# Kernel optimization log

Measured on AMD Instinct MI355X. Metric: run time of the kernel, lower is better.

Reference implementation:

```python
import jax, jax.numpy as jnp
import numpy as np

N_NODES = 50000
N_EDGES = 800000
D = 64


def setup_inputs() -> dict:
    key = jax.random.key(0)
    ks = jax.random.split(key, 8)
    x = jax.random.normal(ks[0], (N_NODES, D), dtype=jnp.float32)
    edge_index = jax.random.randint(ks[1], (2, N_EDGES), 0, N_NODES, dtype=jnp.int64)
    # GCNConv params (PyG: Linear without bias inside lin, bias added after aggregation)
    def glorot(k, fan_in, fan_out):
        lim = (6.0 / (fan_in + fan_out)) ** 0.5
        return jax.random.uniform(k, (fan_in, fan_out), jnp.float32, -lim, lim)
    W1 = glorot(ks[2], D, D); b1 = jnp.zeros((D,), jnp.float32)
    W2 = glorot(ks[3], D, D); b2 = jnp.zeros((D,), jnp.float32)
    W3 = glorot(ks[4], D, D); b3 = jnp.zeros((D,), jnp.float32)
    return {"x": x, "edge_index": edge_index,
            "W1": W1, "b1": b1, "W2": W2, "b2": b2, "W3": W3, "b3": b3}


def _gcn_norm(edge_index, n_nodes, dtype):
    # Add self-loops, compute symmetric normalization D^-1/2 (A+I) D^-1/2 (PyG GCNConv default).
    loop = jnp.arange(n_nodes, dtype=edge_index.dtype)
    src = jnp.concatenate([edge_index[0], loop])  # message source j
    dst = jnp.concatenate([edge_index[1], loop])  # aggregation target i
    deg = jax.ops.segment_sum(jnp.ones_like(dst, dtype=dtype), dst, num_segments=n_nodes)
    dinv = jnp.where(deg > 0, jax.lax.rsqrt(deg), 0.0)
    norm = dinv[src] * dinv[dst]  # [E + N]
    return src, dst, norm


def _gcn_conv(x, src, dst, norm, W, b, n_nodes):
    h = x @ W                              # [N, D_out]
    msg = h[src] * norm[:, None]           # gather + scale, [E+N, D_out]
    out = jax.ops.segment_sum(msg, dst, num_segments=n_nodes)  # scatter-add
    return out + b


def reference(x, edge_index, W1, b1, W2, b2, W3, b3):
    n = x.shape[0]
    src, dst, norm = _gcn_norm(edge_index, n, x.dtype)
    # layer 0: conv -> relu -> residual
    h = _gcn_conv(x, src, dst, norm, W1, b1, n)
    h = jax.nn.relu(h) + x
    # layer 1: conv -> relu -> residual
    r = h
    h = _gcn_conv(h, src, dst, norm, W2, b2, n)
    h = jax.nn.relu(h) + r
    # layer 2 (final): conv only
    h = _gcn_conv(h, src, dst, norm, W3, b3, n)
    return h
```

## Files before the change

### kernel.cpp

```cpp
#include <hip/hip_runtime.h>
#include <hip/hip_bf16.h>


#define CAP 64
#define EDGE_CHUNK 1024

typedef __attribute__((ext_vector_type(8))) short bf16x8;
typedef __attribute__((ext_vector_type(4))) float f32x4;

__device__ inline unsigned pack_bf16(float a, float b) {
    union { float f; unsigned i; } ua, ub;
    ua.f = a; ub.f = b;
    unsigned x = (ua.i + 0x7fffu + ((ua.i >> 16) & 1u)) >> 16;
    unsigned y = (ub.i + 0x7fffu + ((ub.i >> 16) & 1u)) >> 16;
    return x | (y << 16);
}
__device__ inline unsigned short to_bf16(float a) {
    union { float f; unsigned i; } u; u.f = a;
    return (unsigned short)((u.i + 0x7fffu + ((u.i >> 16) & 1u)) >> 16);
}
__device__ inline void acc_bf16x2(unsigned u, float& a, float& b) {
    union { unsigned i; float f; } lo, hi;
    lo.i = u << 16;
    hi.i = u & 0xffff0000u;
    a += lo.f; b += hi.f;
}

__global__ void fill_kernel(const int* __restrict__ src, const int* __restrict__ dst,
                            int* __restrict__ cnt, int* __restrict__ adj,
                            int E, int npc) {
    int cls = blockIdx.x & 7;
    int base = (blockIdx.x >> 3) * EDGE_CHUNK;
    int end = min(base + EDGE_CHUNK, E);
    int lo = cls * npc, hi = lo + npc;
    for (int e = base + threadIdx.x; e < end; e += blockDim.x) {
        int d = dst[e];
        if (d >= lo && d < hi) {
            int p = atomicAdd(&cnt[d], 1);
            adj[(size_t)d * CAP + p] = src[e];
        }
    }
}

__global__ __launch_bounds__(256) void gemm_kernel(const float* __restrict__ in,
                                                   const float* __restrict__ W,
                                                   const int* __restrict__ cnt,
                                                   unsigned short* __restrict__ g, int n) {
    __shared__ unsigned short Wb[512 * 8];
    int t = threadIdx.x;

#pragma unroll
    for (int e0 = 0; e0 < 2; e0++) {
        int e = t + e0 * 256;
        int sc = e >> 6;
        int l  = e & 63;
        int s = sc >> 2, c = sc & 3;
        int nn = c * 16 + (l & 15);
        int kb = s * 32 + (l >> 4) * 8;
        const float* wp = &W[(size_t)kb * 64 + nn];
        unsigned q0 = pack_bf16(wp[0 * 64], wp[1 * 64]);
        unsigned q1 = pack_bf16(wp[2 * 64], wp[3 * 64]);
        unsigned q2 = pack_bf16(wp[4 * 64], wp[5 * 64]);
        unsigned q3 = pack_bf16(wp[6 * 64], wp[7 * 64]);
        *(uint4*)&Wb[e * 8] = make_uint4(q0, q1, q2, q3);
    }

    int wv = t >> 6;
    int lane = t & 63;
    int quad = lane >> 4;
    int m16 = lane & 15;

    int rowA = blockIdx.x * 64 + wv * 16 + m16;
    union { bf16x8 v; uint4 u; } a0, a1;
    {
        float4 f0 = make_float4(0, 0, 0, 0), f1 = f0, f2 = f0, f3 = f0;
        if (rowA < n) {
            const float* rp = &in[(size_t)rowA * 64];
            f0 = *(const float4*)&rp[quad * 8];
            f1 = *(const float4*)&rp[quad * 8 + 4];
            f2 = *(const float4*)&rp[32 + quad * 8];
            f3 = *(const float4*)&rp[32 + quad * 8 + 4];
        }
        a0.u = make_uint4(pack_bf16(f0.x, f0.y), pack_bf16(f0.z, f0.w),
                          pack_bf16(f1.x, f1.y), pack_bf16(f1.z, f1.w));
        a1.u = make_uint4(pack_bf16(f2.x, f2.y), pack_bf16(f2.z, f2.w),
                          pack_bf16(f3.x, f3.y), pack_bf16(f3.z, f3.w));
    }
    __syncthreads();

    f32x4 acc[4];
#pragma unroll
    for (int c = 0; c < 4; c++) {
        bf16x8 b0 = *(const bf16x8*)&Wb[((size_t)(0 * 4 + c) * 64 + lane) * 8];
        bf16x8 b1 = *(const bf16x8*)&Wb[((size_t)(1 * 4 + c) * 64 + lane) * 8];
        f32x4 z = {0.f, 0.f, 0.f, 0.f};
        z = __builtin_amdgcn_mfma_f32_16x16x32_bf16(a0.v, b0, z, 0, 0, 0);
        z = __builtin_amdgcn_mfma_f32_16x16x32_bf16(a1.v, b1, z, 0, 0, 0);
        acc[c] = z;
    }

    int rowbase = blockIdx.x * 64 + wv * 16 + quad * 4;
    float dv[4];
#pragma unroll
    for (int r = 0; r < 4; r++) {
        int row = rowbase + r;
        dv[r] = (row < n) ? rsqrtf((float)(cnt[row] + 1)) : 0.f;
    }
#pragma unroll
    for (int c = 0; c < 4; c++) {
#pragma unroll
        for (int r = 0; r < 4; r++) {
            int row = rowbase + r;
            if (row < n)
                g[(size_t)row * 64 + c * 16 + m16] = to_bf16(acc[c][r] * dv[r]);
        }
    }
}

template <int MODE>
__global__ __launch_bounds__(256) void agg_kernel(const unsigned short* __restrict__ g,
                                                  const int* __restrict__ cnt,
                                                  const int* __restrict__ adj,
                                                  const float* __restrict__ bias,
                                                  const float* __restrict__ res,
                                                  float* __restrict__ out, int n) {
    int t = threadIdx.x;
    int lg = t & 7;
    int i = blockIdx.x * 32 + (t >> 3);
    if (i >= n) return;
    int deg = cnt[i];
    const int* lst = adj + (size_t)i * CAP;
    const int c8 = lg * 8;
    size_t rowoff = (size_t)i * 64 + c8;
    float4 r0 = make_float4(0.f, 0.f, 0.f, 0.f), r1 = r0;
    if (MODE == 0) {
        r0 = *(const float4*)&res[rowoff];
        r1 = *(const float4*)&res[rowoff + 4];
    }
    float a0 = 0.f, a1 = 0.f, a2 = 0.f, a3 = 0.f;
    float a4 = 0.f, a5 = 0.f, a6 = 0.f, a7 = 0.f;
    {
        uint4 v = *(const uint4*)&g[(size_t)i * 64 + c8];
        acc_bf16x2(v.x, a0, a1); acc_bf16x2(v.y, a2, a3);
        acc_bf16x2(v.z, a4, a5); acc_bf16x2(v.w, a6, a7);
    }
    int k = 0;
    for (; k + 8 <= deg; k += 8) {
        int4 ja = *(const int4*)&lst[k];
        int4 jb = *(const int4*)&lst[k + 4];
        uint4 v0 = *(const uint4*)&g[(size_t)ja.x * 64 + c8];
        uint4 v1 = *(const uint4*)&g[(size_t)ja.y * 64 + c8];
        uint4 v2 = *(const uint4*)&g[(size_t)ja.z * 64 + c8];
        uint4 v3 = *(const uint4*)&g[(size_t)ja.w * 64 + c8];
        uint4 v4 = *(const uint4*)&g[(size_t)jb.x * 64 + c8];
        uint4 v5 = *(const uint4*)&g[(size_t)jb.y * 64 + c8];
        uint4 v6 = *(const uint4*)&g[(size_t)jb.z * 64 + c8];
        uint4 v7 = *(const uint4*)&g[(size_t)jb.w * 64 + c8];
        acc_bf16x2(v0.x, a0, a1); acc_bf16x2(v0.y, a2, a3);
        acc_bf16x2(v0.z, a4, a5); acc_bf16x2(v0.w, a6, a7);
        acc_bf16x2(v1.x, a0, a1); acc_bf16x2(v1.y, a2, a3);
        acc_bf16x2(v1.z, a4, a5); acc_bf16x2(v1.w, a6, a7);
        acc_bf16x2(v2.x, a0, a1); acc_bf16x2(v2.y, a2, a3);
        acc_bf16x2(v2.z, a4, a5); acc_bf16x2(v2.w, a6, a7);
        acc_bf16x2(v3.x, a0, a1); acc_bf16x2(v3.y, a2, a3);
        acc_bf16x2(v3.z, a4, a5); acc_bf16x2(v3.w, a6, a7);
        acc_bf16x2(v4.x, a0, a1); acc_bf16x2(v4.y, a2, a3);
        acc_bf16x2(v4.z, a4, a5); acc_bf16x2(v4.w, a6, a7);
        acc_bf16x2(v5.x, a0, a1); acc_bf16x2(v5.y, a2, a3);
        acc_bf16x2(v5.z, a4, a5); acc_bf16x2(v5.w, a6, a7);
        acc_bf16x2(v6.x, a0, a1); acc_bf16x2(v6.y, a2, a3);
        acc_bf16x2(v6.z, a4, a5); acc_bf16x2(v6.w, a6, a7);
        acc_bf16x2(v7.x, a0, a1); acc_bf16x2(v7.y, a2, a3);
        acc_bf16x2(v7.z, a4, a5); acc_bf16x2(v7.w, a6, a7);
    }
    if (k + 4 <= deg) {
        int4 ja = *(const int4*)&lst[k];
        uint4 v0 = *(const uint4*)&g[(size_t)ja.x * 64 + c8];
        uint4 v1 = *(const uint4*)&g[(size_t)ja.y * 64 + c8];
        uint4 v2 = *(const uint4*)&g[(size_t)ja.z * 64 + c8];
        uint4 v3 = *(const uint4*)&g[(size_t)ja.w * 64 + c8];
        acc_bf16x2(v0.x, a0, a1); acc_bf16x2(v0.y, a2, a3);
        acc_bf16x2(v0.z, a4, a5); acc_bf16x2(v0.w, a6, a7);
        acc_bf16x2(v1.x, a0, a1); acc_bf16x2(v1.y, a2, a3);
        acc_bf16x2(v1.z, a4, a5); acc_bf16x2(v1.w, a6, a7);
        acc_bf16x2(v2.x, a0, a1); acc_bf16x2(v2.y, a2, a3);
        acc_bf16x2(v2.z, a4, a5); acc_bf16x2(v2.w, a6, a7);
        acc_bf16x2(v3.x, a0, a1); acc_bf16x2(v3.y, a2, a3);
        acc_bf16x2(v3.z, a4, a5); acc_bf16x2(v3.w, a6, a7);
        k += 4;
    }
    for (; k < deg; k++) {
        uint4 v = *(const uint4*)&g[(size_t)lst[k] * 64 + c8];
        acc_bf16x2(v.x, a0, a1); acc_bf16x2(v.y, a2, a3);
        acc_bf16x2(v.z, a4, a5); acc_bf16x2(v.w, a6, a7);
    }
    float dv = rsqrtf((float)(deg + 1));
    float4 b0 = *(const float4*)&bias[c8];
    float4 b1 = *(const float4*)&bias[c8 + 4];
    float4 o0, o1;
    o0.x = dv * a0 + b0.x; o0.y = dv * a1 + b0.y;
    o0.z = dv * a2 + b0.z; o0.w = dv * a3 + b0.w;
    o1.x = dv * a4 + b1.x; o1.y = dv * a5 + b1.y;
    o1.z = dv * a6 + b1.z; o1.w = dv * a7 + b1.w;
    if (MODE == 0) {
        o0.x = fmaxf(o0.x, 0.f) + r0.x; o0.y = fmaxf(o0.y, 0.f) + r0.y;
        o0.z = fmaxf(o0.z, 0.f) + r0.z; o0.w = fmaxf(o0.w, 0.f) + r0.w;
        o1.x = fmaxf(o1.x, 0.f) + r1.x; o1.y = fmaxf(o1.y, 0.f) + r1.y;
        o1.z = fmaxf(o1.z, 0.f) + r1.z; o1.w = fmaxf(o1.w, 0.f) + r1.w;
    }
    *(float4*)&out[rowoff] = o0;
    *(float4*)&out[rowoff + 4] = o1;
}

extern "C" void kernel_launch(void* const* d_in, const int* in_sizes, int n_in,
                              void* d_out, int out_size, void* d_ws, size_t ws_size,
                              hipStream_t stream) {
    const float* x  = (const float*)d_in[0];
    const int*   ei = (const int*)d_in[1];
    const float* W1 = (const float*)d_in[2];
    const float* b1 = (const float*)d_in[3];
    const float* W2 = (const float*)d_in[4];
    const float* b2 = (const float*)d_in[5];
    const float* W3 = (const float*)d_in[6];
    const float* b3 = (const float*)d_in[7];
    float* out = (float*)d_out;

    const int N = in_sizes[0] / 64;
    const int E = in_sizes[1] / 2;
    const int* src = ei;
    const int* dst = ei + E;
    const int npc = (N + 7) / 8;
    const int nEdgeChunks = (E + EDGE_CHUNK - 1) / EDGE_CHUNK;

    char* p = (char*)d_ws;
    int*            cnt = (int*)p;            p += ((N + 63) / 64) * 64 * 4;
    int*            adj = (int*)p;            p += ((size_t)N + 1) * CAP * 4;
    unsigned short* g   = (unsigned short*)p; p += (size_t)N * 64 * 2;
    float*          h   = (float*)p;          p += (size_t)N * 64 * 4;

    const int aggBlocks  = (N + 31) / 32;
    const int gemmBlocks = (N + 63) / 64;

    hipMemsetAsync(cnt, 0, (size_t)N * 4, stream);
    fill_kernel<<<nEdgeChunks * 8, 256, 0, stream>>>(src, dst, cnt, adj, E, npc);

    gemm_kernel<<<gemmBlocks, 256, 0, stream>>>(x, W1, cnt, g, N);
    agg_kernel<0><<<aggBlocks, 256, 0, stream>>>(g, cnt, adj, b1, x, h, N);

    gemm_kernel<<<gemmBlocks, 256, 0, stream>>>(h, W2, cnt, g, N);
    agg_kernel<0><<<aggBlocks, 256, 0, stream>>>(g, cnt, adj, b2, h, h, N);

    gemm_kernel<<<gemmBlocks, 256, 0, stream>>>(h, W3, cnt, g, N);
    agg_kernel<1><<<aggBlocks, 256, 0, stream>>>(g, cnt, adj, b3, nullptr, out, N);
}
```

Before: 198.4 us.

## Fuse aggregation with the next layer's GEMM via shared-memory MFMA tiles

```diff
diff --git a/kernel.cpp b/kernel.cpp
--- a/kernel.cpp
+++ b/kernel.cpp
@@ -42,13 +42,7 @@
     }
 }
 
-__global__ __launch_bounds__(256) void gemm_kernel(const float* __restrict__ in,
-                                                   const float* __restrict__ W,
-                                                   const int* __restrict__ cnt,
-                                                   unsigned short* __restrict__ g, int n) {
-    __shared__ unsigned short Wb[512 * 8];
-    int t = threadIdx.x;
-
+__device__ inline void stage_W(const float* __restrict__ W, unsigned short* Wb, int t) {
 #pragma unroll
     for (int e0 = 0; e0 < 2; e0++) {
         int e = t + e0 * 256;
@@ -64,6 +58,15 @@
         unsigned q3 = pack_bf16(wp[6 * 64], wp[7 * 64]);
         *(uint4*)&Wb[e * 8] = make_uint4(q0, q1, q2, q3);
     }
+}
+
+__global__ __launch_bounds__(256) void gemm_kernel(const float* __restrict__ in,
+                                                   const float* __restrict__ W,
+                                                   const int* __restrict__ cnt,
+                                                   unsigned short* __restrict__ g, int n) {
+    __shared__ unsigned short Wb[512 * 8];
+    int t = threadIdx.x;
+    stage_W(W, Wb, t);
 
     int wv = t >> 6;
     int lane = t & 63;
@@ -117,12 +120,135 @@
     }
 }
 
-template <int MODE>
+template <int WRITE_H>
+__global__ __launch_bounds__(256) void aggemm_kernel(
+        const unsigned short* __restrict__ g_in,
+        const int* __restrict__ cnt,
+        const int* __restrict__ adj,
+        const float* __restrict__ bias,
+        const float* __restrict__ res,
+        const float* __restrict__ W,
+        float* __restrict__ h_out,
+        unsigned short* __restrict__ g_out,
+        int n) {
+    __shared__ unsigned short Wb[512 * 8];
+    __shared__ unsigned short Afrag[512 * 8];
+    int t = threadIdx.x;
+    stage_W(W, Wb, t);
+
+    int np = t >> 4;
+    int lg = t & 15;
+    const int c4 = lg * 4;
+    int chunk = lg >> 1;
+    int half  = lg & 1;
+#pragma unroll 1
+    for (int p = 0; p < 4; p++) {
+        int i = blockIdx.x * 64 + p * 16 + np;
+        float vx = 0.f, vy = 0.f, vz = 0.f, vw = 0.f;
+        if (i < n) {
+            int deg = cnt[i];
+            const int* lst = adj + (size_t)i * CAP;
+            float4 rr = *(const float4*)&res[(size_t)i * 64 + c4];
+            float ax = 0.f, ay = 0.f, az = 0.f, aw = 0.f;
+            {
+                uint2 v = *(const uint2*)&g_in[(size_t)i * 64 + c4];
+                acc_bf16x2(v.x, ax, ay);
+                acc_bf16x2(v.y, az, aw);
+            }
+            int k = 0;
+            for (; k + 8 <= deg; k += 8) {
+                int4 ja = *(const int4*)&lst[k];
+                int4 jb = *(const int4*)&lst[k + 4];
+                uint2 v0 = *(const uint2*)&g_in[(size_t)ja.x * 64 + c4];
+                uint2 v1 = *(const uint2*)&g_in[(size_t)ja.y * 64 + c4];
+                uint2 v2 = *(const uint2*)&g_in[(size_t)ja.z * 64 + c4];
+                uint2 v3 = *(const uint2*)&g_in[(size_t)ja.w * 64 + c4];
+                uint2 v4 = *(const uint2*)&g_in[(size_t)jb.x * 64 + c4];
+                uint2 v5 = *(const uint2*)&g_in[(size_t)jb.y * 64 + c4];
+                uint2 v6 = *(const uint2*)&g_in[(size_t)jb.z * 64 + c4];
+                uint2 v7 = *(const uint2*)&g_in[(size_t)jb.w * 64 + c4];
+                acc_bf16x2(v0.x, ax, ay); acc_bf16x2(v0.y, az, aw);
+                acc_bf16x2(v1.x, ax, ay); acc_bf16x2(v1.y, az, aw);
+                acc_bf16x2(v2.x, ax, ay); acc_bf16x2(v2.y, az, aw);
+                acc_bf16x2(v3.x, ax, ay); acc_bf16x2(v3.y, az, aw);
+                acc_bf16x2(v4.x, ax, ay); acc_bf16x2(v4.y, az, aw);
+                acc_bf16x2(v5.x, ax, ay); acc_bf16x2(v5.y, az, aw);
+                acc_bf16x2(v6.x, ax, ay); acc_bf16x2(v6.y, az, aw);
+                acc_bf16x2(v7.x, ax, ay); acc_bf16x2(v7.y, az, aw);
+            }
+            if (k + 4 <= deg) {
+                int4 ja = *(const int4*)&lst[k];
+                uint2 v0 = *(const uint2*)&g_in[(size_t)ja.x * 64 + c4];
+                uint2 v1 = *(const uint2*)&g_in[(size_t)ja.y * 64 + c4];
+                uint2 v2 = *(const uint2*)&g_in[(size_t)ja.z * 64 + c4];
+                uint2 v3 = *(const uint2*)&g_in[(size_t)ja.w * 64 + c4];
+                acc_bf16x2(v0.x, ax, ay); acc_bf16x2(v0.y, az, aw);
+                acc_bf16x2(v1.x, ax, ay); acc_bf16x2(v1.y, az, aw);
+                acc_bf16x2(v2.x, ax, ay); acc_bf16x2(v2.y, az, aw);
+                acc_bf16x2(v3.x, ax, ay); acc_bf16x2(v3.y, az, aw);
+                k += 4;
+            }
+            for (; k < deg; k++) {
+                uint2 v = *(const uint2*)&g_in[(size_t)lst[k] * 64 + c4];
+                acc_bf16x2(v.x, ax, ay);
+                acc_bf16x2(v.y, az, aw);
+            }
+            float dvv = rsqrtf((float)(deg + 1));
+            float4 bb = *(const float4*)&bias[c4];
+            vx = fmaxf(dvv * ax + bb.x, 0.f) + rr.x;
+            vy = fmaxf(dvv * ay + bb.y, 0.f) + rr.y;
+            vz = fmaxf(dvv * az + bb.z, 0.f) + rr.z;
+            vw = fmaxf(dvv * aw + bb.w, 0.f) + rr.w;
+            if (WRITE_H) {
+                float4 hv = make_float4(vx, vy, vz, vw);
+                *(float4*)&h_out[(size_t)i * 64 + c4] = hv;
+            }
+        }
+        uint2 pk;
+        pk.x = pack_bf16(vx, vy);
+        pk.y = pack_bf16(vz, vw);
+        *(uint2*)&Afrag[(((size_t)(p * 8 + chunk) * 16 + np) * 8) + half * 4] = pk;
+    }
+    __syncthreads();
+
+    int wv = t >> 6;
+    int lane = t & 63;
+    int quad = lane >> 4;
+    int m16 = lane & 15;
+    bf16x8 a0 = *(const bf16x8*)&Afrag[((size_t)(wv * 8 + quad) * 16 + m16) * 8];
+    bf16x8 a1 = *(const bf16x8*)&Afrag[((size_t)(wv * 8 + 4 + quad) * 16 + m16) * 8];
+    f32x4 acc[4];
+#pragma unroll
+    for (int c = 0; c < 4; c++) {
+        bf16x8 b0 = *(const bf16x8*)&Wb[((size_t)(0 * 4 + c) * 64 + lane) * 8];
+        bf16x8 b1 = *(const bf16x8*)&Wb[((size_t)(1 * 4 + c) * 64 + lane) * 8];
+        f32x4 z = {0.f, 0.f, 0.f, 0.f};
+        z = __builtin_amdgcn_mfma_f32_16x16x32_bf16(a0, b0, z, 0, 0, 0);
+        z = __builtin_amdgcn_mfma_f32_16x16x32_bf16(a1, b1, z, 0, 0, 0);
+        acc[c] = z;
+    }
+    int rowbase = blockIdx.x * 64 + wv * 16 + quad * 4;
+    float dv2[4];
+#pragma unroll
+    for (int r = 0; r < 4; r++) {
+        int row = rowbase + r;
+        dv2[r] = (row < n) ? rsqrtf((float)(cnt[row] + 1)) : 0.f;
+    }
+#pragma unroll
+    for (int c = 0; c < 4; c++) {
+#pragma unroll
+        for (int r = 0; r < 4; r++) {
+            int row = rowbase + r;
+            if (row < n)
+                g_out[(size_t)row * 64 + c * 16 + m16] = to_bf16(acc[c][r] * dv2[r]);
+        }
+    }
+}
+
 __global__ __launch_bounds__(256) void agg_kernel(const unsigned short* __restrict__ g,
                                                   const int* __restrict__ cnt,
                                                   const int* __restrict__ adj,
                                                   const float* __restrict__ bias,
-                                                  const float* __restrict__ res,
                                                   float* __restrict__ out, int n) {
     int t = threadIdx.x;
     int lg = t & 7;
@@ -132,11 +258,6 @@
     const int* lst = adj + (size_t)i * CAP;
     const int c8 = lg * 8;
     size_t rowoff = (size_t)i * 64 + c8;
-    float4 r0 = make_float4(0.f, 0.f, 0.f, 0.f), r1 = r0;
-    if (MODE == 0) {
-        r0 = *(const float4*)&res[rowoff];
-        r1 = *(const float4*)&res[rowoff + 4];
-    }
     float a0 = 0.f, a1 = 0.f, a2 = 0.f, a3 = 0.f;
     float a4 = 0.f, a5 = 0.f, a6 = 0.f, a7 = 0.f;
     {
@@ -202,12 +323,6 @@
     o0.z = dv * a2 + b0.z; o0.w = dv * a3 + b0.w;
     o1.x = dv * a4 + b1.x; o1.y = dv * a5 + b1.y;
     o1.z = dv * a6 + b1.z; o1.w = dv * a7 + b1.w;
-    if (MODE == 0) {
-        o0.x = fmaxf(o0.x, 0.f) + r0.x; o0.y = fmaxf(o0.y, 0.f) + r0.y;
-        o0.z = fmaxf(o0.z, 0.f) + r0.z; o0.w = fmaxf(o0.w, 0.f) + r0.w;
-        o1.x = fmaxf(o1.x, 0.f) + r1.x; o1.y = fmaxf(o1.y, 0.f) + r1.y;
-        o1.z = fmaxf(o1.z, 0.f) + r1.z; o1.w = fmaxf(o1.w, 0.f) + r1.w;
-    }
     *(float4*)&out[rowoff] = o0;
     *(float4*)&out[rowoff + 4] = o1;
 }
@@ -235,21 +350,18 @@
     char* p = (char*)d_ws;
     int*            cnt = (int*)p;            p += ((N + 63) / 64) * 64 * 4;
     int*            adj = (int*)p;            p += ((size_t)N + 1) * CAP * 4;
-    unsigned short* g   = (unsigned short*)p; p += (size_t)N * 64 * 2;
-    float*          h   = (float*)p;          p += (size_t)N * 64 * 4;
-
+    unsigned short* ga  = (unsigned short*)p; p += (size_t)N * 64 * 2;
+    unsigned short* gb  = (unsigned short*)p; p += (size_t)N * 64 * 2;
+    float*          h1  = (float*)p;          p += (size_t)N * 64 * 4;
+
+    const int tileBlocks = (N + 63) / 64;
     const int aggBlocks  = (N + 31) / 32;
-    const int gemmBlocks = (N + 63) / 64;
 
     hipMemsetAsync(cnt, 0, (size_t)N * 4, stream);
     fill_kernel<<<nEdgeChunks * 8, 256, 0, stream>>>(src, dst, cnt, adj, E, npc);
 
-    gemm_kernel<<<gemmBlocks, 256, 0, stream>>>(x, W1, cnt, g, N);
-    agg_kernel<0><<<aggBlocks, 256, 0, stream>>>(g, cnt, adj, b1, x, h, N);
-
-    gemm_kernel<<<gemmBlocks, 256, 0, stream>>>(h, W2, cnt, g, N);
-    agg_kernel<0><<<aggBlocks, 256, 0, stream>>>(g, cnt, adj, b2, h, h, N);
-
-    gemm_kernel<<<gemmBlocks, 256, 0, stream>>>(h, W3, cnt, g, N);
-    agg_kernel<1><<<aggBlocks, 256, 0, stream>>>(g, cnt, adj, b3, nullptr, out, N);
-}
+    gemm_kernel<<<tileBlocks, 256, 0, stream>>>(x, W1, cnt, ga, N);
+    aggemm_kernel<1><<<tileBlocks, 256, 0, stream>>>(ga, cnt, adj, b1, x, W2, h1, gb, N);
+    aggemm_kernel<0><<<tileBlocks, 256, 0, stream>>>(gb, cnt, adj, b2, h1, W3, nullptr, ga, N);
+    agg_kernel<<<aggBlocks, 256, 0, stream>>>(ga, cnt, adj, b3, out, N);
+}
```

Result: no change. 195.5 us (-1.5%).
